# Kernel optimization log

Measured on AMD Instinct MI355X. Metric: run time of the kernel, lower is better.

Reference implementation:

```python
import jax, jax.numpy as jnp
import numpy as np

B, N, F_DIM = 32, 1024, 128
ALPHA = 0.2        # LeakyReLU negative slope
PAD = -9e15        # pad_sequence padding value in the original
DENSITY = 0.05


def setup_inputs() -> dict:
    key = jax.random.key(0)
    k1, k2, k3 = jax.random.split(key, 3)
    # sparse 0/1 adjacency with self-loops so every node has degree >= 1
    adj = (jax.random.uniform(k1, (B, N, N)) < DENSITY).astype(jnp.float32)
    eye = jnp.eye(N, dtype=jnp.float32)[None, :, :]
    adj = jnp.maximum(adj, eye)
    feats = jax.random.normal(k2, (B, N, F_DIM), dtype=jnp.float32)
    # xavier_uniform with leaky_relu gain on a [2F, 1]
    gain = float(np.sqrt(2.0 / (1.0 + ALPHA ** 2)))
    bound = gain * float(np.sqrt(6.0 / (2 * F_DIM + 1)))
    a = jax.random.uniform(k3, (2 * F_DIM, 1), minval=-bound, maxval=bound,
                           dtype=jnp.float32)
    return {"batch_graphs": adj, "batch_features": feats, "a": a}


def reference(batch_graphs, batch_features, a):
    # e_ij = LeakyReLU([h_i || h_j] @ a) decomposes as (h_i @ a1) + (h_j @ a2)
    s_src = batch_features @ a[:F_DIM, 0]   # [B, N] contribution of node i
    s_dst = batch_features @ a[F_DIM:, 0]   # [B, N] contribution of neighbor j
    e = s_src[:, :, None] + s_dst[:, None, :]            # [B, N, N]
    e = jnp.where(e >= 0, e, ALPHA * e)                   # LeakyReLU
    mask = batch_graphs == 1
    e = jnp.where(mask, e, PAD)                           # pad non-edges like pad_sequence
    att = jax.nn.softmax(e, axis=-1)                      # segmented softmax over neighbors
    att = jnp.where(mask, att, 0.0)                       # scatter back only real edges
    return att
```

## Files before the change

kernel.cpp:

```cpp
#include <hip/hip_runtime.h>
#include <hip/hip_bf16.h>
#include <stdint.h>

#define B_DIM 32
#define N_DIM 1024
#define F_DIM 128
#define ALPHA 0.2f
#define NROWS (B_DIM * N_DIM)
#define TAIL_ROWS 128
#define MAIN_ROWS (NROWS - TAIL_ROWS)
#define SCORE_BYTES ((size_t)(2 * NROWS) * sizeof(float))
#define RPW 2

typedef float          vf4 __attribute__((ext_vector_type(4)));
typedef unsigned short vh4 __attribute__((ext_vector_type(4)));
typedef unsigned int   vu4 __attribute__((ext_vector_type(4)));

__device__ __forceinline__ unsigned short f32_to_bf16_bits(float f) {
    union { __hip_bfloat16 h; unsigned short u; } cvt;
    cvt.h = __float2bfloat16(f);
    return cvt.u;
}

__device__ __forceinline__ bool probe_is_f32(const void* adj) {
    return *(const uint32_t*)adj == 0x3F800000u;
}

template <bool F32>
__device__ __forceinline__ float* score_base(void* out) {
    const size_t out_bytes = (size_t)NROWS * N_DIM * (F32 ? 4 : 2);
    return (float*)((char*)out + out_bytes - SCORE_BYTES);
}

__device__ __forceinline__ float leaky(float t) { return fmaxf(t, ALPHA * t); }

template <bool F32>
__device__ __forceinline__ void scores_body(
    const void* __restrict__ feats_v, const void* __restrict__ a_v, void* out)
{
    float* base  = score_base<F32>(out);
    float* s_src = base;
    float* s_dst = base + NROWS;

    const int wid  = threadIdx.x >> 6;
    const int lane = threadIdx.x & 63;
    const int row  = blockIdx.x * 4 + wid;
    const int f0   = lane * 2;

    float x0, x1, a10, a11, a20, a21;
    if (F32) {
        const float* fp = (const float*)feats_v + (size_t)row * F_DIM + f0;
        const float* ap = (const float*)a_v;
        x0 = fp[0]; x1 = fp[1];
        a10 = ap[f0];         a11 = ap[f0 + 1];
        a20 = ap[F_DIM + f0]; a21 = ap[F_DIM + f0 + 1];
    } else {
        const __hip_bfloat16* fp = (const __hip_bfloat16*)feats_v + (size_t)row * F_DIM + f0;
        const __hip_bfloat16* ap = (const __hip_bfloat16*)a_v;
        x0  = __bfloat162float(fp[0]);           x1  = __bfloat162float(fp[1]);
        a10 = __bfloat162float(ap[f0]);          a11 = __bfloat162float(ap[f0 + 1]);
        a20 = __bfloat162float(ap[F_DIM + f0]);  a21 = __bfloat162float(ap[F_DIM + f0 + 1]);
    }

    float v1 = x0 * a10 + x1 * a11;
    float v2 = x0 * a20 + x1 * a21;
    #pragma unroll
    for (int off = 32; off > 0; off >>= 1) {
        v1 += __shfl_down(v1, off, 64);
        v2 += __shfl_down(v2, off, 64);
    }
    if (lane == 0) { s_src[row] = v1; s_dst[row] = v2; }
}

__global__ __launch_bounds__(256) void scores_kernel(
    const void* __restrict__ adj, const void* __restrict__ feats,
    const void* __restrict__ a, void* out)
{
    if (probe_is_f32(adj)) scores_body<true>(feats, a, out);
    else                   scores_body<false>(feats, a, out);
}

template <bool F32>
__device__ __forceinline__ void main_body(const void* __restrict__ adj_v, void* out_v)
{
    const int wid  = threadIdx.x >> 6;
    const int lane = threadIdx.x & 63;
    const int row0 = (blockIdx.x * 4 + wid) * RPW;
    const int b    = row0 >> 10;

    const float* base = score_base<F32>(out_v);
    const float* sdst = base + NROWS + (size_t)b * N_DIM;

    vf4 sd[4];
    #pragma unroll
    for (int c = 0; c < 4; ++c) sd[c] = ((const vf4*)sdst)[c * 64 + lane];

    float ssrc[RPW];
    #pragma unroll
    for (int r = 0; r < RPW; ++r) ssrc[r] = base[row0 + r];

    float p[RPW][16];
    float lsum[RPW];
    #pragma unroll
    for (int r = 0; r < RPW; ++r) lsum[r] = 0.0f;

    #pragma unroll
    for (int r = 0; r < RPW; ++r) {
        #pragma unroll
        for (int c = 0; c < 4; ++c) {
            const int idx = c * 64 + lane;
            const float sdk[4] = {sd[c].x, sd[c].y, sd[c].z, sd[c].w};
            bool v[4];
            if (F32) {
                const vu4 av = ((const vu4*)((const float*)adj_v + (size_t)(row0 + r) * N_DIM))[idx];
                v[0] = av.x != 0u; v[1] = av.y != 0u; v[2] = av.z != 0u; v[3] = av.w != 0u;
            } else {
                const vh4 av = ((const vh4*)((const __hip_bfloat16*)adj_v + (size_t)(row0 + r) * N_DIM))[idx];
                v[0] = av.x != 0; v[1] = av.y != 0; v[2] = av.z != 0; v[3] = av.w != 0;
            }
            #pragma unroll
            for (int k = 0; k < 4; ++k) {
                const float q = v[k] ? __expf(leaky(ssrc[r] + sdk[k])) : 0.0f;
                p[r][c*4+k] = q;
                lsum[r] += q;
            }
        }
    }

    #pragma unroll
    for (int off = 1; off < 64; off <<= 1) {
        #pragma unroll
        for (int r = 0; r < RPW; ++r)
            lsum[r] += __shfl_xor(lsum[r], off, 64);
    }

    #pragma unroll
    for (int r = 0; r < RPW; ++r) {
        const float inv = 1.0f / lsum[r];
        #pragma unroll
        for (int c = 0; c < 4; ++c) {
            const int idx = c * 64 + lane;
            if (F32) {
                vf4 o;
                o.x = p[r][c*4+0] * inv; o.y = p[r][c*4+1] * inv;
                o.z = p[r][c*4+2] * inv; o.w = p[r][c*4+3] * inv;
                ((vf4*)((float*)out_v + (size_t)(row0 + r) * N_DIM))[idx] = o;
            } else {
                vh4 o;
                o.x = f32_to_bf16_bits(p[r][c*4+0] * inv);
                o.y = f32_to_bf16_bits(p[r][c*4+1] * inv);
                o.z = f32_to_bf16_bits(p[r][c*4+2] * inv);
                o.w = f32_to_bf16_bits(p[r][c*4+3] * inv);
                ((vh4*)((__hip_bfloat16*)out_v + (size_t)(row0 + r) * N_DIM))[idx] = o;
            }
        }
    }
}

__global__ __launch_bounds__(256) void main_kernel(
    const void* __restrict__ adj, void* out)
{
    if (probe_is_f32(adj)) main_body<true>(adj, out);
    else                   main_body<false>(adj, out);
}

template <bool F32>
__device__ __forceinline__ void wave_softmax_row(
    const void* __restrict__ adj_v, void* __restrict__ out_v,
    int row, float ssrc, const float* __restrict__ sdst)
{
    const int lane = threadIdx.x & 63;

    float p[16];
    float lsum = 0.0f;

    #pragma unroll
    for (int c = 0; c < 4; ++c) {
        const int idx = c * 64 + lane;
        const vf4 sd = ((const vf4*)sdst)[idx];
        const float sdk[4] = {sd.x, sd.y, sd.z, sd.w};
        bool v[4];
        if (F32) {
            const vu4 av = ((const vu4*)((const float*)adj_v + (size_t)row * N_DIM))[idx];
            v[0] = av.x != 0u; v[1] = av.y != 0u; v[2] = av.z != 0u; v[3] = av.w != 0u;
        } else {
            const vh4 av = ((const vh4*)((const __hip_bfloat16*)adj_v + (size_t)row * N_DIM))[idx];
            v[0] = av.x != 0; v[1] = av.y != 0; v[2] = av.z != 0; v[3] = av.w != 0;
        }
        #pragma unroll
        for (int k = 0; k < 4; ++k) {
            const float q = v[k] ? __expf(leaky(ssrc + sdk[k])) : 0.0f;
            p[c*4+k] = q;
            lsum += q;
        }
    }

    #pragma unroll
    for (int off = 1; off < 64; off <<= 1)
        lsum += __shfl_xor(lsum, off, 64);
    const float inv = 1.0f / lsum;

    #pragma unroll
    for (int c = 0; c < 4; ++c) {
        const int idx = c * 64 + lane;
        if (F32) {
            vf4 o;
            o.x = p[c*4+0] * inv; o.y = p[c*4+1] * inv;
            o.z = p[c*4+2] * inv; o.w = p[c*4+3] * inv;
            ((vf4*)((float*)out_v + (size_t)row * N_DIM))[idx] = o;
        } else {
            vh4 o;
            o.x = f32_to_bf16_bits(p[c*4+0] * inv);
            o.y = f32_to_bf16_bits(p[c*4+1] * inv);
            o.z = f32_to_bf16_bits(p[c*4+2] * inv);
            o.w = f32_to_bf16_bits(p[c*4+3] * inv);
            ((vh4*)((__hip_bfloat16*)out_v + (size_t)row * N_DIM))[idx] = o;
        }
    }
}

template <bool F32>
__device__ __forceinline__ void tail_body(
    const void* __restrict__ adj_v, const void* __restrict__ feats_v,
    const void* __restrict__ a_v, void* __restrict__ out_v)
{
    __shared__ float sdst_sh[N_DIM];

    const int tid  = threadIdx.x;
    const int wid  = tid >> 6;
    const int lane = tid & 63;
    const int b    = B_DIM - 1;
    const int row  = MAIN_ROWS + blockIdx.x * 4 + wid;

    #pragma unroll
    for (int k = 0; k < 4; ++k) {
        const int j = tid * 4 + k;
        float acc = 0.0f;
        if (F32) {
            const vf4* fp = (const vf4*)((const float*)feats_v + ((size_t)b * N_DIM + j) * F_DIM);
            const vf4* ap = (const vf4*)((const float*)a_v + F_DIM);
            #pragma unroll 8
            for (int f = 0; f < F_DIM / 4; ++f) {
                const vf4 x = fp[f], w = ap[f];
                acc += x.x * w.x + x.y * w.y + x.z * w.z + x.w * w.w;
            }
        } else {
            const __hip_bfloat16* fp = (const __hip_bfloat16*)feats_v + ((size_t)b * N_DIM + j) * F_DIM;
            const __hip_bfloat16* ap = (const __hip_bfloat16*)a_v + F_DIM;
            #pragma unroll 8
            for (int f = 0; f < F_DIM; ++f)
                acc += __bfloat162float(fp[f]) * __bfloat162float(ap[f]);
        }
        sdst_sh[j] = acc;
    }

    float ssrc;
    {
        const int f0 = lane * 2;
        float x0, x1, a0, a1;
        if (F32) {
            const float* fp = (const float*)feats_v + (size_t)row * F_DIM + f0;
            const float* ap = (const float*)a_v;
            x0 = fp[0]; x1 = fp[1]; a0 = ap[f0]; a1 = ap[f0 + 1];
        } else {
            const __hip_bfloat16* fp = (const __hip_bfloat16*)feats_v + (size_t)row * F_DIM + f0;
            const __hip_bfloat16* ap = (const __hip_bfloat16*)a_v;
            x0 = __bfloat162float(fp[0]); x1 = __bfloat162float(fp[1]);
            a0 = __bfloat162float(ap[f0]); a1 = __bfloat162float(ap[f0 + 1]);
        }
        float v = x0 * a0 + x1 * a1;
        #pragma unroll
        for (int off = 32; off > 0; off >>= 1)
            v += __shfl_down(v, off, 64);
        ssrc = __shfl(v, 0, 64);
    }
    __syncthreads();

    wave_softmax_row<F32>(adj_v, out_v, row, ssrc, sdst_sh);
}

__global__ __launch_bounds__(256) void tail_kernel(
    const void* __restrict__ adj, const void* __restrict__ feats,
    const void* __restrict__ a, void* __restrict__ out)
{
    if (probe_is_f32(adj)) tail_body<true>(adj, feats, a, out);
    else                   tail_body<false>(adj, feats, a, out);
}

extern "C" void kernel_launch(void* const* d_in, const int* in_sizes, int n_in,
                              void* d_out, int out_size, void* d_ws, size_t ws_size,
                              hipStream_t stream) {
    const void* adj   = d_in[0];
    const void* feats = d_in[1];
    const void* a     = d_in[2];
    (void)d_ws; (void)ws_size;

    scores_kernel<<<NROWS / 4, 256, 0, stream>>>(adj, feats, a, d_out);
    main_kernel<<<MAIN_ROWS / (4 * RPW), 256, 0, stream>>>(adj, d_out);
    tail_kernel<<<TAIL_ROWS / 4, 256, 0, stream>>>(adj, feats, a, d_out);
}
```

Baseline: 266.1 us.

## Process eight rows per wave with double-buffered adjacency loads and exp recompute

Each wave in the main kernel now handles a chunk of eight rows sequentially, prefetching the next row's adjacency into a second register buffer while computing the current row. Instead of keeping the exponentials in registers, it recomputes them in the normalisation pass to cut register pressure. The tail kernel inlines the former helper with no behaviour change. Fewer waves and blocks mean less parallelism for hiding latency, and the extra exp work adds compute, in exchange for overlapping loads with computation inside each wave.

```diff
diff --git a/kernel.cpp b/kernel.cpp
--- a/kernel.cpp
+++ b/kernel.cpp
@@ -10,7 +10,7 @@
 #define TAIL_ROWS 128
 #define MAIN_ROWS (NROWS - TAIL_ROWS)
 #define SCORE_BYTES ((size_t)(2 * NROWS) * sizeof(float))
-#define RPW 2
+#define CHUNK 8
 
 typedef float          vf4 __attribute__((ext_vector_type(4)));
 typedef unsigned short vh4 __attribute__((ext_vector_type(4)));
@@ -81,11 +81,24 @@
 }
 
 template <bool F32>
-__device__ __forceinline__ void main_body(const void* __restrict__ adj_v, void* out_v)
+__device__ __forceinline__ void load_adj_row(
+    const void* __restrict__ adj_v, int row, int lane, vu4* u, vh4* h)
+{
+    #pragma unroll
+    for (int c = 0; c < 4; ++c) {
+        const int idx = c * 64 + lane;
+        if (F32) u[c] = ((const vu4*)((const float*)adj_v + (size_t)row * N_DIM))[idx];
+        else     h[c] = ((const vh4*)((const __hip_bfloat16*)adj_v + (size_t)row * N_DIM))[idx];
+    }
+}
+
+template <bool F32>
+__device__ __forceinline__ void main_body(const void* __restrict__ adj_v, void* __restrict__ out_v)
 {
     const int wid  = threadIdx.x >> 6;
     const int lane = threadIdx.x & 63;
-    const int row0 = (blockIdx.x * 4 + wid) * RPW;
+    const int wave = blockIdx.x * 4 + wid;
+    const int row0 = wave * CHUNK;
     const int b    = row0 >> 10;
 
     const float* base = score_base<F32>(out_v);
@@ -95,63 +108,60 @@
     #pragma unroll
     for (int c = 0; c < 4; ++c) sd[c] = ((const vf4*)sdst)[c * 64 + lane];
 
-    float ssrc[RPW];
-    #pragma unroll
-    for (int r = 0; r < RPW; ++r) ssrc[r] = base[row0 + r];
-
-    float p[RPW][16];
-    float lsum[RPW];
-    #pragma unroll
-    for (int r = 0; r < RPW; ++r) lsum[r] = 0.0f;
-
-    #pragma unroll
-    for (int r = 0; r < RPW; ++r) {
+    vu4 au[2][4]; vh4 ah[2][4];
+    load_adj_row<F32>(adj_v, row0, lane, au[0], ah[0]);
+
+    #pragma unroll
+    for (int i = 0; i < CHUNK; ++i) {
+        const int row = row0 + i;
+        const int cur = i & 1;
+        const int nxt = cur ^ 1;
+        if (i + 1 < CHUNK)
+            load_adj_row<F32>(adj_v, row + 1, lane, au[nxt], ah[nxt]);
+
+        const float ssrc = base[row];
+
+        bool v[16];
         #pragma unroll
         for (int c = 0; c < 4; ++c) {
-            const int idx = c * 64 + lane;
+            if (F32) {
+                v[c*4+0] = au[cur][c].x != 0u; v[c*4+1] = au[cur][c].y != 0u;
+                v[c*4+2] = au[cur][c].z != 0u; v[c*4+3] = au[cur][c].w != 0u;
+            } else {
+                v[c*4+0] = ah[cur][c].x != 0;  v[c*4+1] = ah[cur][c].y != 0;
+                v[c*4+2] = ah[cur][c].z != 0;  v[c*4+3] = ah[cur][c].w != 0;
+            }
+        }
+
+        float lsum = 0.0f;
+        #pragma unroll
+        for (int c = 0; c < 4; ++c) {
             const float sdk[4] = {sd[c].x, sd[c].y, sd[c].z, sd[c].w};
-            bool v[4];
-            if (F32) {
-                const vu4 av = ((const vu4*)((const float*)adj_v + (size_t)(row0 + r) * N_DIM))[idx];
-                v[0] = av.x != 0u; v[1] = av.y != 0u; v[2] = av.z != 0u; v[3] = av.w != 0u;
-            } else {
-                const vh4 av = ((const vh4*)((const __hip_bfloat16*)adj_v + (size_t)(row0 + r) * N_DIM))[idx];
-                v[0] = av.x != 0; v[1] = av.y != 0; v[2] = av.z != 0; v[3] = av.w != 0;
-            }
             #pragma unroll
-            for (int k = 0; k < 4; ++k) {
-                const float q = v[k] ? __expf(leaky(ssrc[r] + sdk[k])) : 0.0f;
-                p[r][c*4+k] = q;
-                lsum[r] += q;
-            }
-        }
-    }
-
-    #pragma unroll
-    for (int off = 1; off < 64; off <<= 1) {
-        #pragma unroll
-        for (int r = 0; r < RPW; ++r)
-            lsum[r] += __shfl_xor(lsum[r], off, 64);
-    }
-
-    #pragma unroll
-    for (int r = 0; r < RPW; ++r) {
-        const float inv = 1.0f / lsum[r];
+            for (int k = 0; k < 4; ++k)
+                lsum += v[c*4+k] ? __expf(leaky(ssrc + sdk[k])) : 0.0f;
+        }
+        #pragma unroll
+        for (int off = 1; off < 64; off <<= 1)
+            lsum += __shfl_xor(lsum, off, 64);
+        const float inv = 1.0f / lsum;
+
         #pragma unroll
         for (int c = 0; c < 4; ++c) {
+            const float sdk[4] = {sd[c].x, sd[c].y, sd[c].z, sd[c].w};
+            float q[4];
+            #pragma unroll
+            for (int k = 0; k < 4; ++k)
+                q[k] = v[c*4+k] ? __expf(leaky(ssrc + sdk[k])) * inv : 0.0f;
             const int idx = c * 64 + lane;
             if (F32) {
-                vf4 o;
-                o.x = p[r][c*4+0] * inv; o.y = p[r][c*4+1] * inv;
-                o.z = p[r][c*4+2] * inv; o.w = p[r][c*4+3] * inv;
-                ((vf4*)((float*)out_v + (size_t)(row0 + r) * N_DIM))[idx] = o;
+                vf4 o; o.x = q[0]; o.y = q[1]; o.z = q[2]; o.w = q[3];
+                ((vf4*)((float*)out_v + (size_t)row * N_DIM))[idx] = o;
             } else {
                 vh4 o;
-                o.x = f32_to_bf16_bits(p[r][c*4+0] * inv);
-                o.y = f32_to_bf16_bits(p[r][c*4+1] * inv);
-                o.z = f32_to_bf16_bits(p[r][c*4+2] * inv);
-                o.w = f32_to_bf16_bits(p[r][c*4+3] * inv);
-                ((vh4*)((__hip_bfloat16*)out_v + (size_t)(row0 + r) * N_DIM))[idx] = o;
+                o.x = f32_to_bf16_bits(q[0]); o.y = f32_to_bf16_bits(q[1]);
+                o.z = f32_to_bf16_bits(q[2]); o.w = f32_to_bf16_bits(q[3]);
+                ((vh4*)((__hip_bfloat16*)out_v + (size_t)row * N_DIM))[idx] = o;
             }
         }
     }
@@ -162,61 +172,6 @@
 {
     if (probe_is_f32(adj)) main_body<true>(adj, out);
     else                   main_body<false>(adj, out);
-}
-
-template <bool F32>
-__device__ __forceinline__ void wave_softmax_row(
-    const void* __restrict__ adj_v, void* __restrict__ out_v,
-    int row, float ssrc, const float* __restrict__ sdst)
-{
-    const int lane = threadIdx.x & 63;
-
-    float p[16];
-    float lsum = 0.0f;
-
-    #pragma unroll
-    for (int c = 0; c < 4; ++c) {
-        const int idx = c * 64 + lane;
-        const vf4 sd = ((const vf4*)sdst)[idx];
-        const float sdk[4] = {sd.x, sd.y, sd.z, sd.w};
-        bool v[4];
-        if (F32) {
-            const vu4 av = ((const vu4*)((const float*)adj_v + (size_t)row * N_DIM))[idx];
-            v[0] = av.x != 0u; v[1] = av.y != 0u; v[2] = av.z != 0u; v[3] = av.w != 0u;
-        } else {
-            const vh4 av = ((const vh4*)((const __hip_bfloat16*)adj_v + (size_t)row * N_DIM))[idx];
-            v[0] = av.x != 0; v[1] = av.y != 0; v[2] = av.z != 0; v[3] = av.w != 0;
-        }
-        #pragma unroll
-        for (int k = 0; k < 4; ++k) {
-            const float q = v[k] ? __expf(leaky(ssrc + sdk[k])) : 0.0f;
-            p[c*4+k] = q;
-            lsum += q;
-        }
-    }
-
-    #pragma unroll
-    for (int off = 1; off < 64; off <<= 1)
-        lsum += __shfl_xor(lsum, off, 64);
-    const float inv = 1.0f / lsum;
-
-    #pragma unroll
-    for (int c = 0; c < 4; ++c) {
-        const int idx = c * 64 + lane;
-        if (F32) {
-            vf4 o;
-            o.x = p[c*4+0] * inv; o.y = p[c*4+1] * inv;
-            o.z = p[c*4+2] * inv; o.w = p[c*4+3] * inv;
-            ((vf4*)((float*)out_v + (size_t)row * N_DIM))[idx] = o;
-        } else {
-            vh4 o;
-            o.x = f32_to_bf16_bits(p[c*4+0] * inv);
-            o.y = f32_to_bf16_bits(p[c*4+1] * inv);
-            o.z = f32_to_bf16_bits(p[c*4+2] * inv);
-            o.w = f32_to_bf16_bits(p[c*4+3] * inv);
-            ((vh4*)((__hip_bfloat16*)out_v + (size_t)row * N_DIM))[idx] = o;
-        }
-    }
 }
 
 template <bool F32>
@@ -268,15 +223,57 @@
             x0 = __bfloat162float(fp[0]); x1 = __bfloat162float(fp[1]);
             a0 = __bfloat162float(ap[f0]); a1 = __bfloat162float(ap[f0 + 1]);
         }
-        float v = x0 * a0 + x1 * a1;
+        float s = x0 * a0 + x1 * a1;
         #pragma unroll
         for (int off = 32; off > 0; off >>= 1)
-            v += __shfl_down(v, off, 64);
-        ssrc = __shfl(v, 0, 64);
+            s += __shfl_down(s, off, 64);
+        ssrc = __shfl(s, 0, 64);
     }
     __syncthreads();
 
-    wave_softmax_row<F32>(adj_v, out_v, row, ssrc, sdst_sh);
+    float p[16], lsum = 0.0f;
+    #pragma unroll
+    for (int c = 0; c < 4; ++c) {
+        const int idx = c * 64 + lane;
+        const vf4 sd = ((const vf4*)sdst_sh)[idx];
+        const float sdk[4] = {sd.x, sd.y, sd.z, sd.w};
+        bool v[4];
+        if (F32) {
+            const vu4 av = ((const vu4*)((const float*)adj_v + (size_t)row * N_DIM))[idx];
+            v[0] = av.x != 0u; v[1] = av.y != 0u; v[2] = av.z != 0u; v[3] = av.w != 0u;
+        } else {
+            const vh4 av = ((const vh4*)((const __hip_bfloat16*)adj_v + (size_t)row * N_DIM))[idx];
+            v[0] = av.x != 0; v[1] = av.y != 0; v[2] = av.z != 0; v[3] = av.w != 0;
+        }
+        #pragma unroll
+        for (int k = 0; k < 4; ++k) {
+            const float q = v[k] ? __expf(leaky(ssrc + sdk[k])) : 0.0f;
+            p[c*4+k] = q;
+            lsum += q;
+        }
+    }
+    #pragma unroll
+    for (int off = 1; off < 64; off <<= 1)
+        lsum += __shfl_xor(lsum, off, 64);
+    const float inv = 1.0f / lsum;
+
+    #pragma unroll
+    for (int c = 0; c < 4; ++c) {
+        const int idx = c * 64 + lane;
+        if (F32) {
+            vf4 o;
+            o.x = p[c*4+0] * inv; o.y = p[c*4+1] * inv;
+            o.z = p[c*4+2] * inv; o.w = p[c*4+3] * inv;
+            ((vf4*)((float*)out_v + (size_t)row * N_DIM))[idx] = o;
+        } else {
+            vh4 o;
+            o.x = f32_to_bf16_bits(p[c*4+0] * inv);
+            o.y = f32_to_bf16_bits(p[c*4+1] * inv);
+            o.z = f32_to_bf16_bits(p[c*4+2] * inv);
+            o.w = f32_to_bf16_bits(p[c*4+3] * inv);
+            ((vh4*)((__hip_bfloat16*)out_v + (size_t)row * N_DIM))[idx] = o;
+        }
+    }
 }
 
 __global__ __launch_bounds__(256) void tail_kernel(
@@ -296,6 +293,6 @@
     (void)d_ws; (void)ws_size;
 
     scores_kernel<<<NROWS / 4, 256, 0, stream>>>(adj, feats, a, d_out);
-    main_kernel<<<MAIN_ROWS / (4 * RPW), 256, 0, stream>>>(adj, d_out);
+    main_kernel<<<MAIN_ROWS / (CHUNK * 4), 256, 0, stream>>>(adj, d_out);
     tail_kernel<<<TAIL_ROWS / 4, 256, 0, stream>>>(adj, feats, a, d_out);
 }
```

Measured after the change: 269.7 us. About the same (+1.3%).
